# Kernel optimization log

Measured on AMD Instinct MI355X. Metric: run time of the kernel, lower is better.

Reference implementation:

```python
import jax, jax.numpy as jnp
import numpy as np

B, C, L, E = 8192, 45, 21, 22  # batch, channels, seq_len, num selected channels (45//2)


def setup_inputs() -> dict:
    key = jax.random.key(0)
    ks = jax.random.split(key, 15)
    f = lambda k, s: jax.random.normal(k, s, dtype=jnp.float32) * 0.1
    return {
        "x": jax.random.normal(ks[0], (B, C, L), dtype=jnp.float32),
        # group_conv: Conv1d(1, 21, kernel=21) -> weight (out=21, k=21), bias (21,)
        "gc_w": f(ks[1], (21, 21)),
        "gc_b": f(ks[2], (21,)),
        # mlp: Linear(45,25) -> Tanh -> Linear(25,45) -> Tanh
        "w1": f(ks[3], (25, 45)), "b1": f(ks[4], (25,)),
        "w2": f(ks[5], (45, 25)), "b2": f(ks[6], (45,)),
        # 22 Self_atten experts; all convs are 1x1 so weights reduce to vectors
        "wq": f(ks[7], (E, 21)), "bq": f(ks[8], (E, 21)),
        "wk": f(ks[9], (E, 21)), "bk": f(ks[10], (E, 21)),
        "wv": f(ks[11], (E, 21)), "bv": f(ks[12], (E, 21)),
        "wo": f(ks[13], (E, 21)), "bo": f(ks[14], (E,)),
    }


def reference(x, gc_w, gc_b, w1, b1, w2, b2, wq, bq, wk, bk, wv, bv, wo, bo):
    # --- gating: per-channel conv (kernel==length -> 1 output position) ---
    # temp[b,i,o] = sum_l gc_w[o,l] * x[b,i,l] + gc_b[o]
    temp = jnp.einsum('bil,ol->bio', x, gc_w) + gc_b            # (B, 45, 21)
    mx = temp.max(axis=-1)                                      # maxpool over 21 conv channels
    av = temp.mean(axis=-1)                                     # avgpool over 21 conv channels
    mlp = lambda h: jnp.tanh(jnp.tanh(h @ w1.T + b1) @ w2.T + b2)
    gate = jax.nn.softmax(mlp(mx) + mlp(av), axis=1)            # (B, 45)

    # --- routing: top-22 channels by batch-mean gate (torch detaches the mean) ---
    mean_gate = jax.lax.stop_gradient(gate).mean(axis=0)        # (45,)
    _, top_idx = jax.lax.top_k(mean_gate, E)
    sel = jnp.sort(top_idx)  # experts assigned in ascending channel order

    # --- batched Self_atten over the 22 selected channels ---
    xs = x[:, sel, :].transpose(1, 0, 2)                        # (E, B, L)
    q = wq[:, None, None, :] * xs[..., None] + bq[:, None, None, :]   # (E,B,L,21)
    k = wk[:, None, :, None] * xs[:, :, None, :] + bk[:, None, :, None]  # (E,B,21,L)
    v = wv[:, None, :, None] * xs[:, :, None, :] + bv[:, None, :, None]  # (E,B,21,L)
    energy = jnp.einsum('eblc,ebcm->eblm', q, k)                # (E,B,L,L)
    attn = jax.nn.softmax(energy, axis=-1)
    out = jnp.einsum('ebcm,eblm->ebcl', v, attn)                # (E,B,21,L)
    y = jnp.einsum('ec,ebcl->ebl', wo, out) + bo[:, None, None] # (E,B,L)

    routed = y.transpose(1, 0, 2) * gate[:, sel][:, :, None]    # (B,E,L)
    A = jnp.zeros_like(x).at[:, sel, :].set(routed)             # non-selected channels -> 0

    A_flat = A.reshape(A.shape[0], C * L)
    G = x.reshape(x.shape[0], C * L) * A_flat
    return G, A_flat
```

## Files before the change

kernel.cpp:

```cpp
#include <hip/hip_runtime.h>
#include <float.h>
#include <math.h>

#define BATCH   8192
#define NCH     45
#define SEQL    21
#define NEXP    22
#define ROWLEN  945
#define GOFF    7741440
#define K1_BLOCKS 2048
#define K3_BLOCKS 4096
#define LOG2E   1.4426950408889634f

__device__ __forceinline__ float fast_tanh(float v) {
    const float t = __expf(2.f * v);
    return (t - 1.f) / (t + 1.f);
}

__device__ __forceinline__ float fexp2(float v) {
#if defined(__has_builtin)
#if __has_builtin(__builtin_amdgcn_exp2f)
    return __builtin_amdgcn_exp2f(v);
#else
    return __expf(v * 0.6931471805599453f);
#endif
#else
    return __expf(v * 0.6931471805599453f);
#endif
}

__global__ __launch_bounds__(256) void k1_gate(
    const float* __restrict__ x,
    const float* __restrict__ gc_w, const float* __restrict__ gc_b,
    const float* __restrict__ w1,   const float* __restrict__ b1,
    const float* __restrict__ w2,   const float* __restrict__ b2,
    float* __restrict__ gate_out,   float* __restrict__ partialsT)
{
    __shared__ float xsh[4 * ROWLEN];
    __shared__ float b45a[4][45];
    __shared__ float b45b[4][45];
    __shared__ float b25a[4][25];
    __shared__ float b25b[4][25];

    const int tid  = threadIdx.x;
    const int w    = tid >> 6;
    const int lane = tid & 63;
    const int b_base = blockIdx.x * 4;

    {
        const float4* x4 = (const float4*)(x + (size_t)b_base * ROWLEN);
        float4* xsh4 = (float4*)xsh;
        for (int q = tid; q < 945; q += 256) xsh4[q] = x4[q];
    }
    __syncthreads();

    float g = 0.f;
    if (lane < NCH) {
        float xr[SEQL];
        const float* xp = &xsh[w * ROWLEN + lane * SEQL];
        #pragma unroll
        for (int l = 0; l < SEQL; ++l) xr[l] = xp[l];
        float mx = -FLT_MAX, av = 0.f;
        for (int o = 0; o < SEQL; ++o) {
            float t = gc_b[o];
            #pragma unroll
            for (int l = 0; l < SEQL; ++l) t = fmaf(gc_w[o * SEQL + l], xr[l], t);
            mx = fmaxf(mx, t);
            av += t;
        }
        av *= (1.f / 21.f);
        b45a[w][lane] = mx;
        b45b[w][lane] = av;
    }
    __syncthreads();
    if (lane < 25) {
        float tm = b1[lane], ta = b1[lane];
        for (int i = 0; i < NCH; ++i) {
            const float wv_ = w1[lane * NCH + i];
            tm = fmaf(wv_, b45a[w][i], tm);
            ta = fmaf(wv_, b45b[w][i], ta);
        }
        b25a[w][lane] = fast_tanh(tm);
        b25b[w][lane] = fast_tanh(ta);
    }
    __syncthreads();
    if (lane < NCH) {
        float tm = b2[lane], ta = b2[lane];
        for (int j = 0; j < 25; ++j) {
            const float wv_ = w2[lane * 25 + j];
            tm = fmaf(wv_, b25a[w][j], tm);
            ta = fmaf(wv_, b25b[w][j], ta);
        }
        g = __expf(fast_tanh(tm) + fast_tanh(ta));
        b45a[w][lane] = g;
    }
    __syncthreads();
    if (lane < NCH) {
        float s = 0.f;
        for (int i = 0; i < NCH; ++i) s += b45a[w][i];
        const float gt = g / s;
        gate_out[(size_t)(b_base + w) * NCH + lane] = gt;
        b45b[w][lane] = gt;
    }
    __syncthreads();
    if (tid < NCH) {
        partialsT[tid * K1_BLOCKS + blockIdx.x] =
            b45b[0][tid] + b45b[1][tid] + b45b[2][tid] + b45b[3][tid];
    }
}

__global__ __launch_bounds__(256) void k2_reduce(
    const float* __restrict__ partialsT,
    const float* __restrict__ wq, const float* __restrict__ bq,
    const float* __restrict__ wk, const float* __restrict__ bk,
    const float* __restrict__ wv, const float* __restrict__ bv,
    const float* __restrict__ wo, const float* __restrict__ bo,
    float* __restrict__ mg, float* __restrict__ escal)
{
    const int tid = threadIdx.x;
    const int c   = blockIdx.x;

    if (c < NCH) {
        __shared__ float wsum[4];
        const float4* p4 = (const float4*)(partialsT + c * K1_BLOCKS);
        const float4 v0 = p4[tid];
        const float4 v1 = p4[tid + 256];
        float s = ((v0.x + v0.y) + (v0.z + v0.w)) + ((v1.x + v1.y) + (v1.z + v1.w));
        #pragma unroll
        for (int off = 32; off > 0; off >>= 1) s += __shfl_xor(s, off, 64);
        if ((tid & 63) == 0) wsum[tid >> 6] = s;
        __syncthreads();
        if (tid == 0) mg[c] = (wsum[0] + wsum[1]) + (wsum[2] + wsum[3]);
    } else {
        if (tid < NEXP) {
            const int e = tid;
            float A = 0.f, Cc = 0.f, P = 0.f, Q = 0.f;
            for (int i = 0; i < SEQL; ++i) {
                A  = fmaf(wq[e * SEQL + i], wk[e * SEQL + i], A);
                Cc = fmaf(bq[e * SEQL + i], wk[e * SEQL + i], Cc);
                P  = fmaf(wo[e * SEQL + i], wv[e * SEQL + i], P);
                Q  = fmaf(wo[e * SEQL + i], bv[e * SEQL + i], Q);
            }
            Q += bo[e];
            escal[e]      = A  * LOG2E;
            escal[22 + e] = Cc * LOG2E;
            escal[44 + e] = P;
            escal[66 + e] = Q;
        }
    }
}

__global__ __launch_bounds__(256) void k3_attn(
    const float* __restrict__ x, const float* __restrict__ gate,
    const float* __restrict__ mg, const float* __restrict__ escal,
    float* __restrict__ out)
{
    __shared__ float xsh[2 * ROWLEN];
    __shared__ float ash[2 * ROWLEN];
    __shared__ float smg[64];
    __shared__ float gat[2][NEXP];
    __shared__ float sA[NEXP], sC[NEXP], sP[NEXP], sQ[NEXP];
    __shared__ int   ssel[NEXP];

    const int tid = threadIdx.x;

    if (tid < 64) smg[tid] = (tid < NCH) ? mg[tid] : -FLT_MAX;
    if (tid >= 64 && tid < 64 + NEXP) {
        const int e = tid - 64;
        sA[e] = escal[e];       sC[e] = escal[22 + e];
        sP[e] = escal[44 + e];  sQ[e] = escal[66 + e];
    }

    const int b0 = blockIdx.x * 2;
    {
        const float2* x2 = (const float2*)(x + (size_t)b0 * ROWLEN);
        float2* xsh2 = (float2*)xsh;
        float2* ash2 = (float2*)ash;
        const float2 z = make_float2(0.f, 0.f);
        for (int q = tid; q < 945; q += 256) {
            xsh2[q] = x2[q];
            ash2[q] = z;
        }
    }
    __syncthreads();

    if (tid < 64) {
        const float v = smg[tid];
        int rank = 0;
        #pragma unroll
        for (int i = 0; i < NCH; ++i) {
            const float u = smg[i];
            rank += (u > v || (u == v && i < tid)) ? 1 : 0;
        }
        const bool seld = (tid < NCH) && (rank < NEXP);
        const unsigned long long m = __ballot(seld);
        if (seld) {
            const int e = __popcll(m & ((1ull << tid) - 1ull));
            ssel[e] = tid;
        }
    }
    __syncthreads();

    if (tid < 2 * NEXP) {
        const int bi = (tid >= NEXP) ? 1 : 0;
        const int e  = tid - bi * NEXP;
        gat[bi][e] = gate[(size_t)(b0 + bi) * NCH + ssel[e]];
    }
    __syncthreads();

    {
        const int t0 = (tid * 924) >> 8;
        const int t1 = ((tid + 1) * 924) >> 8;
        int cur_be = -1;
        float xr[SEQL];
        float Ae = 0.f, Ce = 0.f, Pe = 0.f, Qe = 0.f, ge = 0.f;
        const float* xp = nullptr;
        float* ap = nullptr;

        for (int tsk = t0; tsk < t1; ++tsk) {
            const int be = (tsk * 3121) >> 16;
            if (be != cur_be) {
                cur_be = be;
                const int bi = (be * 2979) >> 16;
                const int e  = be - bi * NEXP;
                xp = &xsh[bi * ROWLEN + ssel[e] * SEQL];
                ap = &ash[bi * ROWLEN + ssel[e] * SEQL];
                #pragma unroll
                for (int m = 0; m < SEQL; ++m) xr[m] = xp[m];
                Ae = sA[e]; Ce = sC[e]; Pe = sP[e]; Qe = sQ[e];
                ge = gat[bi][e];
            }
            const int l = tsk - cur_be * SEQL;
            const float al2 = fmaf(Ae, xp[l], Ce);
            float den = 0.f, num = 0.f;
            #pragma unroll
            for (int m = 0; m < SEQL; ++m) {
                const float wgt = fexp2(al2 * xr[m]);
                den += wgt;
                num = fmaf(xr[m], wgt, num);
            }
            ap[l] = fmaf(Pe, __fdividef(num, den), Qe) * ge;
        }
    }
    __syncthreads();

    {
        const float2* xsh2 = (const float2*)xsh;
        const float2* ash2 = (const float2*)ash;
        float2* g2 = (float2*)out + (size_t)blockIdx.x * 945;
        float2* a2 = (float2*)(out + (size_t)GOFF) + (size_t)blockIdx.x * 945;
        for (int q = tid; q < 945; q += 256) {
            const float2 a = ash2[q];
            const float2 xv = xsh2[q];
            g2[q] = make_float2(a.x * xv.x, a.y * xv.y);
            a2[q] = a;
        }
    }
}

extern "C" void kernel_launch(void* const* d_in, const int* in_sizes, int n_in,
                              void* d_out, int out_size, void* d_ws, size_t ws_size,
                              hipStream_t stream)
{
    const float* x    = (const float*)d_in[0];
    const float* gc_w = (const float*)d_in[1];
    const float* gc_b = (const float*)d_in[2];
    const float* w1   = (const float*)d_in[3];
    const float* b1   = (const float*)d_in[4];
    const float* w2   = (const float*)d_in[5];
    const float* b2   = (const float*)d_in[6];
    const float* wq   = (const float*)d_in[7];
    const float* bq   = (const float*)d_in[8];
    const float* wk   = (const float*)d_in[9];
    const float* bk   = (const float*)d_in[10];
    const float* wv   = (const float*)d_in[11];
    const float* bv   = (const float*)d_in[12];
    const float* wo   = (const float*)d_in[13];
    const float* bo   = (const float*)d_in[14];

    float* ws        = (float*)d_ws;
    float* partialsT = ws;
    float* mg        = ws + 92160;
    float* escal     = ws + 92224;
    float* gateBuf   = ws + 92352;
    float* outF      = (float*)d_out;

    k1_gate<<<dim3(K1_BLOCKS), dim3(256), 0, stream>>>(x, gc_w, gc_b, w1, b1, w2, b2,
                                                       gateBuf, partialsT);
    k2_reduce<<<dim3(46), dim3(256), 0, stream>>>(partialsT, wq, bq, wk, bk, wv, bv,
                                                  wo, bo, mg, escal);
    k3_attn<<<dim3(K3_BLOCKS), dim3(256), 0, stream>>>(x, gateBuf, mg, escal, outF);
}
```

Measured before the change: 151.5 us.

## Drop reduce kernel via slotted atomics, shuffle-based gate MLP, nontemporal output stores

Removes the separate reduction kernel. Gate partial sums are now accumulated with atomicAdd into 8 slots per channel, which needs a memset first, and each k3 block folds those slots and recomputes the per-expert scalars itself. The gate MLP in k1 now passes values between lanes with wave shuffles instead of shared memory and block barriers. Final output writes use nontemporal stores. This trades one kernel launch and several barriers for atomic contention, redundant per-block scalar work, and summation order that is no longer deterministic.

```diff
diff --git a/kernel.cpp b/kernel.cpp
--- a/kernel.cpp
+++ b/kernel.cpp
@@ -10,7 +10,10 @@
 #define GOFF    7741440
 #define K1_BLOCKS 2048
 #define K3_BLOCKS 4096
+#define NSLOT   8
 #define LOG2E   1.4426950408889634f
+
+typedef float vfloat2 __attribute__((ext_vector_type(2)));
 
 __device__ __forceinline__ float fast_tanh(float v) {
     const float t = __expf(2.f * v);
@@ -34,13 +37,10 @@
     const float* __restrict__ gc_w, const float* __restrict__ gc_b,
     const float* __restrict__ w1,   const float* __restrict__ b1,
     const float* __restrict__ w2,   const float* __restrict__ b2,
-    float* __restrict__ gate_out,   float* __restrict__ partialsT)
+    float* __restrict__ gate_out,   float* __restrict__ mg8)
 {
     __shared__ float xsh[4 * ROWLEN];
-    __shared__ float b45a[4][45];
-    __shared__ float b45b[4][45];
-    __shared__ float b25a[4][25];
-    __shared__ float b25b[4][25];
+    __shared__ float part[4][NCH];
 
     const int tid  = threadIdx.x;
     const int w    = tid >> 6;
@@ -54,105 +54,63 @@
     }
     __syncthreads();
 
-    float g = 0.f;
-    if (lane < NCH) {
-        float xr[SEQL];
-        const float* xp = &xsh[w * ROWLEN + lane * SEQL];
+    const int ch = (lane < NCH) ? lane : (NCH - 1);
+    float xr[SEQL];
+    {
+        const float* xp = &xsh[w * ROWLEN + ch * SEQL];
         #pragma unroll
         for (int l = 0; l < SEQL; ++l) xr[l] = xp[l];
-        float mx = -FLT_MAX, av = 0.f;
-        for (int o = 0; o < SEQL; ++o) {
-            float t = gc_b[o];
-            #pragma unroll
-            for (int l = 0; l < SEQL; ++l) t = fmaf(gc_w[o * SEQL + l], xr[l], t);
-            mx = fmaxf(mx, t);
-            av += t;
-        }
-        av *= (1.f / 21.f);
-        b45a[w][lane] = mx;
-        b45b[w][lane] = av;
-    }
-    __syncthreads();
-    if (lane < 25) {
-        float tm = b1[lane], ta = b1[lane];
-        for (int i = 0; i < NCH; ++i) {
-            const float wv_ = w1[lane * NCH + i];
-            tm = fmaf(wv_, b45a[w][i], tm);
-            ta = fmaf(wv_, b45b[w][i], ta);
-        }
-        b25a[w][lane] = fast_tanh(tm);
-        b25b[w][lane] = fast_tanh(ta);
-    }
-    __syncthreads();
+    }
+    float mx = -FLT_MAX, av = 0.f;
+    for (int o = 0; o < SEQL; ++o) {
+        float t = gc_b[o];
+        #pragma unroll
+        for (int l = 0; l < SEQL; ++l) t = fmaf(gc_w[o * SEQL + l], xr[l], t);
+        mx = fmaxf(mx, t);
+        av += t;
+    }
+    av *= (1.f / 21.f);
+
+    const int jj = (lane < 25) ? lane : 24;
+    float tm = b1[jj], ta = b1[jj];
+    for (int i = 0; i < NCH; ++i) {
+        const float wv_ = w1[jj * NCH + i];
+        tm = fmaf(wv_, __shfl(mx, i, 64), tm);
+        ta = fmaf(wv_, __shfl(av, i, 64), ta);
+    }
+    const float hm = fast_tanh(tm);
+    const float ha = fast_tanh(ta);
+
+    float tm2 = b2[ch], ta2 = b2[ch];
+    for (int j = 0; j < 25; ++j) {
+        const float wv_ = w2[ch * 25 + j];
+        tm2 = fmaf(wv_, __shfl(hm, j, 64), tm2);
+        ta2 = fmaf(wv_, __shfl(ha, j, 64), ta2);
+    }
+    float g = (lane < NCH) ? __expf(fast_tanh(tm2) + fast_tanh(ta2)) : 0.f;
+    float s = g;
+    #pragma unroll
+    for (int off = 32; off > 0; off >>= 1) s += __shfl_xor(s, off, 64);
+    const float gt = g / s;
+
     if (lane < NCH) {
-        float tm = b2[lane], ta = b2[lane];
-        for (int j = 0; j < 25; ++j) {
-            const float wv_ = w2[lane * 25 + j];
-            tm = fmaf(wv_, b25a[w][j], tm);
-            ta = fmaf(wv_, b25b[w][j], ta);
-        }
-        g = __expf(fast_tanh(tm) + fast_tanh(ta));
-        b45a[w][lane] = g;
-    }
-    __syncthreads();
-    if (lane < NCH) {
-        float s = 0.f;
-        for (int i = 0; i < NCH; ++i) s += b45a[w][i];
-        const float gt = g / s;
         gate_out[(size_t)(b_base + w) * NCH + lane] = gt;
-        b45b[w][lane] = gt;
+        part[w][lane] = gt;
     }
     __syncthreads();
     if (tid < NCH) {
-        partialsT[tid * K1_BLOCKS + blockIdx.x] =
-            b45b[0][tid] + b45b[1][tid] + b45b[2][tid] + b45b[3][tid];
-    }
-}
-
-__global__ __launch_bounds__(256) void k2_reduce(
-    const float* __restrict__ partialsT,
+        atomicAdd(&mg8[tid * NSLOT + (blockIdx.x & (NSLOT - 1))],
+                  part[0][tid] + part[1][tid] + part[2][tid] + part[3][tid]);
+    }
+}
+
+__global__ __launch_bounds__(256) void k3_attn(
+    const float* __restrict__ x, const float* __restrict__ gate,
+    const float* __restrict__ mg8,
     const float* __restrict__ wq, const float* __restrict__ bq,
     const float* __restrict__ wk, const float* __restrict__ bk,
     const float* __restrict__ wv, const float* __restrict__ bv,
     const float* __restrict__ wo, const float* __restrict__ bo,
-    float* __restrict__ mg, float* __restrict__ escal)
-{
-    const int tid = threadIdx.x;
-    const int c   = blockIdx.x;
-
-    if (c < NCH) {
-        __shared__ float wsum[4];
-        const float4* p4 = (const float4*)(partialsT + c * K1_BLOCKS);
-        const float4 v0 = p4[tid];
-        const float4 v1 = p4[tid + 256];
-        float s = ((v0.x + v0.y) + (v0.z + v0.w)) + ((v1.x + v1.y) + (v1.z + v1.w));
-        #pragma unroll
-        for (int off = 32; off > 0; off >>= 1) s += __shfl_xor(s, off, 64);
-        if ((tid & 63) == 0) wsum[tid >> 6] = s;
-        __syncthreads();
-        if (tid == 0) mg[c] = (wsum[0] + wsum[1]) + (wsum[2] + wsum[3]);
-    } else {
-        if (tid < NEXP) {
-            const int e = tid;
-            float A = 0.f, Cc = 0.f, P = 0.f, Q = 0.f;
-            for (int i = 0; i < SEQL; ++i) {
-                A  = fmaf(wq[e * SEQL + i], wk[e * SEQL + i], A);
-                Cc = fmaf(bq[e * SEQL + i], wk[e * SEQL + i], Cc);
-                P  = fmaf(wo[e * SEQL + i], wv[e * SEQL + i], P);
-                Q  = fmaf(wo[e * SEQL + i], bv[e * SEQL + i], Q);
-            }
-            Q += bo[e];
-            escal[e]      = A  * LOG2E;
-            escal[22 + e] = Cc * LOG2E;
-            escal[44 + e] = P;
-            escal[66 + e] = Q;
-        }
-    }
-}
-
-__global__ __launch_bounds__(256) void k3_attn(
-    const float* __restrict__ x, const float* __restrict__ gate,
-    const float* __restrict__ mg, const float* __restrict__ escal,
     float* __restrict__ out)
 {
     __shared__ float xsh[2 * ROWLEN];
@@ -163,15 +121,8 @@
     __shared__ int   ssel[NEXP];
 
     const int tid = threadIdx.x;
-
-    if (tid < 64) smg[tid] = (tid < NCH) ? mg[tid] : -FLT_MAX;
-    if (tid >= 64 && tid < 64 + NEXP) {
-        const int e = tid - 64;
-        sA[e] = escal[e];       sC[e] = escal[22 + e];
-        sP[e] = escal[44 + e];  sQ[e] = escal[66 + e];
-    }
-
-    const int b0 = blockIdx.x * 2;
+    const int b0  = blockIdx.x * 2;
+
     {
         const float2* x2 = (const float2*)(x + (size_t)b0 * ROWLEN);
         float2* xsh2 = (float2*)xsh;
@@ -181,6 +132,30 @@
             xsh2[q] = x2[q];
             ash2[q] = z;
         }
+    }
+
+    if (tid < 64) {
+        float s = -FLT_MAX;
+        if (tid < NCH) {
+            const float4* p = (const float4*)(mg8 + tid * NSLOT);
+            const float4 a = p[0], b = p[1];
+            s = ((a.x + a.y) + (a.z + a.w)) + ((b.x + b.y) + (b.z + b.w));
+        }
+        smg[tid] = s;
+    }
+    if (tid >= 64 && tid < 64 + NEXP) {
+        const int e = tid - 64;
+        float A = 0.f, Cc = 0.f, P = 0.f, Q = 0.f;
+        for (int i = 0; i < SEQL; ++i) {
+            A  = fmaf(wq[e * SEQL + i], wk[e * SEQL + i], A);
+            Cc = fmaf(bq[e * SEQL + i], wk[e * SEQL + i], Cc);
+            P  = fmaf(wo[e * SEQL + i], wv[e * SEQL + i], P);
+            Q  = fmaf(wo[e * SEQL + i], bv[e * SEQL + i], Q);
+        }
+        sA[e] = A * LOG2E;
+        sC[e] = Cc * LOG2E;
+        sP[e] = P;
+        sQ[e] = Q + bo[e];
     }
     __syncthreads();
 
@@ -245,15 +220,17 @@
     __syncthreads();
 
     {
-        const float2* xsh2 = (const float2*)xsh;
-        const float2* ash2 = (const float2*)ash;
-        float2* g2 = (float2*)out + (size_t)blockIdx.x * 945;
-        float2* a2 = (float2*)(out + (size_t)GOFF) + (size_t)blockIdx.x * 945;
+        const float* xs = xsh;
+        const float* as = ash;
+        vfloat2* g2 = (vfloat2*)out + (size_t)blockIdx.x * 945;
+        vfloat2* a2 = (vfloat2*)(out + (size_t)GOFF) + (size_t)blockIdx.x * 945;
         for (int q = tid; q < 945; q += 256) {
-            const float2 a = ash2[q];
-            const float2 xv = xsh2[q];
-            g2[q] = make_float2(a.x * xv.x, a.y * xv.y);
-            a2[q] = a;
+            const float a0 = as[2 * q],     a1 = as[2 * q + 1];
+            const float x0 = xs[2 * q],     x1 = xs[2 * q + 1];
+            vfloat2 gv; gv.x = a0 * x0; gv.y = a1 * x1;
+            vfloat2 av_; av_.x = a0;    av_.y = a1;
+            __builtin_nontemporal_store(gv, &g2[q]);
+            __builtin_nontemporal_store(av_, &a2[q]);
         }
     }
 }
@@ -278,16 +255,16 @@
     const float* wo   = (const float*)d_in[13];
     const float* bo   = (const float*)d_in[14];
 
-    float* ws        = (float*)d_ws;
-    float* partialsT = ws;
-    float* mg        = ws + 92160;
-    float* escal     = ws + 92224;
-    float* gateBuf   = ws + 92352;
-    float* outF      = (float*)d_out;
+    float* ws      = (float*)d_ws;
+    float* mg8     = ws;
+    float* gateBuf = ws + 384;
+    float* outF    = (float*)d_out;
+
+    (void)hipMemsetAsync(mg8, 0, NCH * NSLOT * sizeof(float), stream);
 
     k1_gate<<<dim3(K1_BLOCKS), dim3(256), 0, stream>>>(x, gc_w, gc_b, w1, b1, w2, b2,
-                                                       gateBuf, partialsT);
-    k2_reduce<<<dim3(46), dim3(256), 0, stream>>>(partialsT, wq, bq, wk, bk, wv, bv,
-                                                  wo, bo, mg, escal);
-    k3_attn<<<dim3(K3_BLOCKS), dim3(256), 0, stream>>>(x, gateBuf, mg, escal, outF);
-}
+                                                       gateBuf, mg8);
+    k3_attn<<<dim3(K3_BLOCKS), dim3(256), 0, stream>>>(x, gateBuf, mg8,
+                                                       wq, bq, wk, bk, wv, bv, wo, bo,
+                                                       outF);
+}
```

Result: slower. 194.6 us (+28.5%).
